# Kernel optimization log

Hardware: AMD Instinct MI355X
Metric: run time of the kernel (lower is better)

Reference implementation:

```python
import jax, jax.numpy as jnp
import numpy as np

N, F_IN, H, OUT, E = 50000, 128, 128, 40, 800000


def setup_inputs() -> dict:
    key = jax.random.key(0)
    ks = jax.random.split(key, 20)
    s = 0.05
    return {
        "x": jax.random.normal(ks[0], (N, F_IN), jnp.float32),
        "edge_index": jax.random.randint(ks[1], (2, E), 0, N, jnp.int64),
        # GATConv (heads=1)
        "W_gat": jax.random.normal(ks[2], (F_IN, H), jnp.float32) * s,
        "att_src": jax.random.normal(ks[3], (H,), jnp.float32) * s,
        "att_dst": jax.random.normal(ks[4], (H,), jnp.float32) * s,
        "b_gat": jnp.zeros((H,), jnp.float32),
        # GCNConv
        "W_gcn": jax.random.normal(ks[5], (F_IN, H), jnp.float32) * s,
        "b_gcn": jnp.zeros((H,), jnp.float32),
        # SAGEConv (mean aggr): lin_l on neighbors (with bias), lin_r on root (no bias)
        "W_sage_l": jax.random.normal(ks[6], (F_IN, H), jnp.float32) * s,
        "b_sage_l": jnp.zeros((H,), jnp.float32),
        "W_sage_r": jax.random.normal(ks[7], (F_IN, H), jnp.float32) * s,
        # MLP head
        "W1": jax.random.normal(ks[8], (3 * H, 2 * H), jnp.float32) * s,
        "b1": jnp.zeros((2 * H,), jnp.float32),
        "W2": jax.random.normal(ks[9], (2 * H, H), jnp.float32) * s,
        "b2": jnp.zeros((H,), jnp.float32),
        "W3": jax.random.normal(ks[10], (H, OUT), jnp.float32) * s,
        "b3": jnp.zeros((OUT,), jnp.float32),
        # BatchNorm1d(3H)
        "gamma": jnp.ones((3 * H,), jnp.float32),
        "beta": jnp.zeros((3 * H,), jnp.float32),
    }


def _add_self_loops(edge_index, n):
    loop = jnp.arange(n, dtype=edge_index.dtype)
    src = jnp.concatenate([edge_index[0], loop])
    dst = jnp.concatenate([edge_index[1], loop])
    return src, dst


def _gat(x, src, dst, n, W, att_src, att_dst, bias):
    h = x @ W                                   # [N, H]
    a_s = h @ att_src                           # [N]
    a_d = h @ att_dst                           # [N]
    e = jax.nn.leaky_relu(a_s[src] + a_d[dst], 0.2)  # [E']
    m = jax.ops.segment_max(e, dst, num_segments=n)
    ex = jnp.exp(e - m[dst])
    denom = jax.ops.segment_sum(ex, dst, num_segments=n)
    alpha = ex / denom[dst]
    out = jax.ops.segment_sum(alpha[:, None] * h[src], dst, num_segments=n)
    return out + bias


def _gcn(x, src, dst, n, W, bias):
    h = x @ W
    deg = jax.ops.segment_sum(jnp.ones_like(dst, dtype=h.dtype), dst, num_segments=n)
    dinv = jnp.where(deg > 0, jax.lax.rsqrt(deg), 0.0)
    norm = dinv[src] * dinv[dst]                # [E']
    out = jax.ops.segment_sum(norm[:, None] * h[src], dst, num_segments=n)
    return out + bias


def _sage(x, src, dst, n, W_l, b_l, W_r):
    agg = jax.ops.segment_sum(x[src], dst, num_segments=n)
    cnt = jax.ops.segment_sum(jnp.ones_like(dst, dtype=x.dtype), dst, num_segments=n)
    mean = agg / jnp.maximum(cnt, 1.0)[:, None]
    return mean @ W_l + b_l + x @ W_r


def reference(x, edge_index, W_gat, att_src, att_dst, b_gat, W_gcn, b_gcn,
              W_sage_l, b_sage_l, W_sage_r, W1, b1, W2, b2, W3, b3, gamma, beta):
    n = x.shape[0]
    src, dst = edge_index[0], edge_index[1]          # SAGE: no self-loops
    src_sl, dst_sl = _add_self_loops(edge_index, n)  # GAT/GCN add self-loops

    x_gat = _gat(x, src_sl, dst_sl, n, W_gat, att_src, att_dst, b_gat)
    x_gcn = _gcn(x, src_sl, dst_sl, n, W_gcn, b_gcn)
    x_sage = _sage(x, src, dst, n, W_sage_l, b_sage_l, W_sage_r)

    h = jnp.concatenate([x_gat, x_gcn, x_sage], axis=1)  # [N, 3H]
    # BatchNorm1d (training-mode batch statistics; biased variance, eps=1e-5)
    mu = h.mean(axis=0)
    var = h.var(axis=0)
    h = (h - mu) * jax.lax.rsqrt(var + 1e-5) * gamma + beta
    # dropout is identity at inference
    h = jax.nn.relu(h) @ W1 + b1
    h = jax.nn.relu(h) @ W2 + b2
    h = jax.nn.relu(h) @ W3 + b3
    return h
```

## Files before the change

kernel.cpp:

```cpp
#include <hip/hip_runtime.h>
#include <cstdint>
#include <cstddef>

#define NN   50000
#define FIN  128
#define HD   128
#define EE   800000
#define C3   384
#define NOUT 40

#define SC_ELEMS 512
#define SC_BLKS  ((NN + SC_ELEMS - 1) / SC_ELEMS)
#define NBLK ((NN + 127) / 128)

#define SPLIT_BLKS ((NN + 4) / 4)

#define NBUCK ((NN + 511) / 512)
#define BCAP  16384
#define BK_BLKS ((EE + 8191) / 8192)
#define SCAP  12288

#define REC_CAP 252
#define ZROW NN

#define LDSW 132

typedef __attribute__((ext_vector_type(8))) short s8v;
typedef __attribute__((ext_vector_type(4))) float f4v;
typedef __attribute__((ext_vector_type(4))) ushort u4v;

typedef const __attribute__((address_space(1))) unsigned int* guintp;
typedef __attribute__((address_space(3))) unsigned int* luintp;

static __device__ __forceinline__ void async_copy16(const void* g, void* l) {
    __builtin_amdgcn_global_load_lds((guintp)g, (luintp)l, 16, 0, 0);
}

static __device__ __forceinline__ float b2f(ushort u) {
    return __uint_as_float((unsigned)u << 16);
}
static __device__ __forceinline__ ushort f2b(float v) {
    unsigned u = __float_as_uint(v);
    unsigned r = u + 0x7fffu + ((u >> 16) & 1u);
    return (ushort)(r >> 16);
}

__global__ __launch_bounds__(256) void k_split_x_att(
    const float* __restrict__ x,
    const float* __restrict__ w_as, const float* __restrict__ w_ad,
    ushort* __restrict__ xb,
    float* __restrict__ a_s, float* __restrict__ a_d)
{
    int node = blockIdx.x * 4 + (threadIdx.x >> 6);
    if (node > NN) return;
    int lane = threadIdx.x & 63;
    size_t o = (size_t)node * 128 + lane * 2;
    if (node == NN) {
        ushort2 z; z.x = 0; z.y = 0;
        *(ushort2*)(xb + o) = z;
        return;
    }
    float2 v  = *(const float2*)(x + o);
    { ushort2 u; u.x = f2b(v.x); u.y = f2b(v.y); *(ushort2*)(xb + o) = u; }
    float2 w1 = *(const float2*)(w_as + lane * 2);
    float2 w2 = *(const float2*)(w_ad + lane * 2);
    float s1 = v.x * w1.x + v.y * w1.y;
    float s2 = v.x * w2.x + v.y * w2.y;
    #pragma unroll
    for (int off = 32; off; off >>= 1) {
        s1 += __shfl_down(s1, off);
        s2 += __shfl_down(s2, off);
    }
    if (lane == 0) { a_s[node] = s1; a_d[node] = s2; }
}

__global__ void k_splitw_all(
    const float* __restrict__ Wg, const float* __restrict__ Wc,
    const float* __restrict__ Wl, const float* __restrict__ Wr,
    const float* __restrict__ W1, const float* __restrict__ W2,
    const float* __restrict__ W3,
    const float* __restrict__ asv, const float* __restrict__ adv,
    float* __restrict__ w_as, float* __restrict__ w_ad,
    ushort* __restrict__ btg, ushort* __restrict__ btc,
    ushort* __restrict__ btsg,
    ushort* __restrict__ bt1, ushort* __restrict__ bt2,
    ushort* __restrict__ bt3)
{
    int ry = blockIdx.x;
    int t = threadIdx.x;
    if (ry == 816) {
        if (t < 128) {
            float s1 = 0.f, s2 = 0.f;
            for (int j = 0; j < 128; ++j) {
                float w = Wg[t * 128 + j];
                s1 += w * asv[j];
                s2 += w * adv[j];
            }
            w_as[t] = s1; w_ad[t] = s2;
        }
        return;
    }
    const float* W = nullptr; ushort* dh; int K, Nw, n;
    bool sage = false;
    if (ry < 128)      { n = ry;       K = 128; Nw = 128; W = Wg; dh = btg; }
    else if (ry < 256) { n = ry - 128; K = 128; Nw = 128; W = Wc; dh = btc; }
    else if (ry < 384) { n = ry - 256; K = 256; Nw = 128; sage = true; dh = btsg; }
    else if (ry < 640) { n = ry - 384; K = 384; Nw = 256; W = W1; dh = bt1; }
    else if (ry < 768) { n = ry - 640; K = 256; Nw = 128; W = W2; dh = bt2; }
    else               { n = ry - 768; K = 128; Nw = 40;  W = W3; dh = bt3; }
    for (int k = t; k < K; k += 256) {
        float v;
        if (sage) v = (k < 128) ? Wl[(size_t)k * 128 + n] : Wr[(size_t)(k - 128) * 128 + n];
        else      v = (n < Nw) ? W[(size_t)k * Nw + n] : 0.f;
        dh[(size_t)n * K + k] = f2b(v);
    }
}

template<int NT, int NCH, int AX>
__global__ __launch_bounds__(256, 5) void k_gemm2(
    const ushort* __restrict__ A, int K,
    const ushort* __restrict__ Bt,
    int M, int mode,
    const float* __restrict__ bias,
    float* __restrict__ Cf, int ldc,
    ushort* __restrict__ Ch, int ldch,
    int colmax)
{
    constexpr int COLS = NT * 16;
    constexpr int HOPU = 8 * COLS;
    constexpr int KTOT = NCH * 128;

    __shared__ __align__(16) ushort S[16384];
    ushort* Bs = S;
    ushort* As = S + 8192;

    const int lane = threadIdx.x & 63;
    const int wave = threadIdx.x >> 6;
    const int quad = lane >> 4;
    const int ln15 = lane & 15;
    const int brow = AX ? blockIdx.y : blockIdx.x;
    const int bcol = AX ? blockIdx.x : blockIdx.y;
    const int row0 = brow * 128 + wave * 32;
    const int col0 = bcol * COLS;
    const int Rbase = brow * 128;

    auto stageB = [&](int c, int h) {
        for (int u0 = wave * 64; u0 < HOPU; u0 += 256) {
            int u  = u0 + lane;
            int kq  = u / COLS;
            int col = u - kq * COLS;
            int kk  = c * 128 + h * 64 + kq * 8;
            const ushort* gp = Bt + (size_t)(col0 + col) * KTOT + kk;
            async_copy16(gp, (char*)Bs + (size_t)u0 * 16);
        }
    };
    auto stageA = [&](int c, int h) {
        #pragma unroll
        for (int i = 0; i < 4; ++i) {
            int u0 = (wave * 4 + i) * 64;
            int u  = u0 + lane;
            int row = u >> 3;
            int s   = u & 7;
            int sg  = s ^ (row & 7);
            int rr = Rbase + row; if (rr > M - 1) rr = M - 1;
            int kk = c * 128 + h * 64 + sg * 8;
            const ushort* gp = A + (size_t)rr * K + kk;
            async_copy16(gp, (char*)As + (size_t)u0 * 16);
        }
    };
    auto afrag = [&](int jj, int mt) -> s8v {
        int r = wave * 32 + mt * 16 + ln15;
        int sg = jj * 4 + quad;
        int unit = r * 8 + (sg ^ (r & 7));
        return *(const s8v*)(As + (size_t)unit * 8);
    };

    f4v acc[2][NT] = {};

    auto compute = [&](int jj) {
        s8v a0 = afrag(jj, 0);
        s8v a1 = afrag(jj, 1);
        #pragma unroll
        for (int t = 0; t < NT; ++t) {
            int ub = (jj * 4 + quad) * COLS + t * 16 + ln15;
            s8v b = *(const s8v*)(Bs + (size_t)ub * 8);
            acc[0][t] = __builtin_amdgcn_mfma_f32_16x16x32_bf16(a0, b, acc[0][t], 0, 0, 0);
            acc[1][t] = __builtin_amdgcn_mfma_f32_16x16x32_bf16(a1, b, acc[1][t], 0, 0, 0);
        }
    };

    stageB(0, 0); stageA(0, 0);
    __syncthreads();

    #pragma unroll
    for (int ph = 0; ph < NCH; ++ph) {
        #pragma unroll
        for (int h = 0; h < 2; ++h) {
            compute(0); compute(1);
            if (!(ph == NCH - 1 && h == 1)) {
                __syncthreads();
                int nc = ph, nh = h + 1;
                if (nh == 2) { nh = 0; ++nc; }
                stageB(nc, nh); stageA(nc, nh);
                __syncthreads();
            }
        }
    }

    if (NT == 8 && mode == 0) {
        __syncthreads();
        ushort* Lp = S + wave * 2176;
        #pragma unroll
        for (int mt = 0; mt < 2; ++mt) {
            #pragma unroll
            for (int t = 0; t < NT; ++t) {
                int cc = col0 + t * 16 + ln15;
                #pragma unroll
                for (int r = 0; r < 4; ++r) {
                    float v = acc[mt][t][r] + bias[cc];
                    v = v > 0.f ? v : 0.f;
                    Lp[(quad * 4 + r) * LDSW + t * 16 + ln15] = f2b(v);
                }
            }
            int cb = (lane & 31) * 4;
            #pragma unroll
            for (int it = 0; it < 8; ++it) {
                int row2 = it * 2 + (lane >> 5);
                int rr = row0 + mt * 16 + row2;
                uint2 v = *(uint2*)(Lp + row2 * LDSW + cb);
                if (rr < M)
                    *(uint2*)(Ch + (size_t)rr * ldch + col0 + cb) = v;
            }
        }
    } else {
        #pragma unroll
        for (int t = 0; t < NT; ++t) {
            int cc = col0 + t * 16 + ln15;
            #pragma unroll
            for (int mt = 0; mt < 2; ++mt) {
                #pragma unroll
                for (int r = 0; r < 4; ++r) {
                    int rr = row0 + mt * 16 + quad * 4 + r;
                    if (rr < M && cc < colmax)
                        Cf[(size_t)rr * ldc + cc] = acc[mt][t][r] + bias[cc];
                }
            }
        }
    }
}

__global__ __launch_bounds__(256, 3) void k_gemm_prod(
    const ushort* __restrict__ tgb, const ushort* __restrict__ tcb,
    const ushort* __restrict__ tsb, const ushort* __restrict__ xb,
    const ushort* __restrict__ btg, const ushort* __restrict__ btc,
    const ushort* __restrict__ btsg,
    const float* __restrict__ bg, const float* __restrict__ bc,
    const float* __restrict__ bsl,
    float* __restrict__ pS, float* __restrict__ pQ,
    ushort* __restrict__ hch)
{
    constexpr int COLS = 128;
    constexpr int HOPU = 8 * COLS;
    __shared__ __align__(16) ushort S[16384];
    ushort* Bs = S;
    ushort* As = S + 8192;
    float* red = (float*)(S + 14336);

    const int z = blockIdx.z;
    const ushort* A1 = (z == 0) ? tgb : (z == 1) ? tcb : tsb;
    const ushort* Bt = (z == 0) ? btg : (z == 1) ? btc : btsg;
    const float*  bias = (z == 0) ? bg : (z == 1) ? bc : bsl;
    const int nch = (z == 2) ? 2 : 1;
    const int ktot = nch * 128;

    const int lane = threadIdx.x & 63;
    const int wave = threadIdx.x >> 6;
    const int quad = lane >> 4;
    const int ln15 = lane & 15;
    const int row0 = blockIdx.x * 128 + wave * 32;
    const int Rbase = blockIdx.x * 128;

    auto stageB = [&](int c, int h) {
        for (int u0 = wave * 64; u0 < HOPU; u0 += 256) {
            int u  = u0 + lane;
            int kq  = u / COLS;
            int col = u - kq * COLS;
            int kk  = c * 128 + h * 64 + kq * 8;
            const ushort* gp = Bt + (size_t)col * ktot + kk;
            async_copy16(gp, (char*)Bs + (size_t)u0 * 16);
        }
    };
    auto stageA = [&](int c, int h) {
        #pragma unroll
        for (int i = 0; i < 4; ++i) {
            int u0 = (wave * 4 + i) * 64;
            int u  = u0 + lane;
            int row = u >> 3;
            int s   = u & 7;
            int sg  = s ^ (row & 7);
            int rr = Rbase + row; if (rr > NN - 1) rr = NN - 1;
            int kk = c * 128 + h * 64 + sg * 8;
            const ushort* gp = (kk < 128) ? (A1 + (size_t)rr * 128 + kk)
                                          : (xb + (size_t)rr * 128 + (kk - 128));
            async_copy16(gp, (char*)As + (size_t)u0 * 16);
        }
    };
    auto afrag = [&](int jj, int mt) -> s8v {
        int r = wave * 32 + mt * 16 + ln15;
        int sg = jj * 4 + quad;
        int unit = r * 8 + (sg ^ (r & 7));
        return *(const s8v*)(As + (size_t)unit * 8);
    };

    f4v acc[2][8] = {};

    auto compute = [&](int jj) {
        s8v a0 = afrag(jj, 0);
        s8v a1 = afrag(jj, 1);
        #pragma unroll
        for (int t = 0; t < 8; ++t) {
            int ub = (jj * 4 + quad) * COLS + t * 16 + ln15;
            s8v b = *(const s8v*)(Bs + (size_t)ub * 8);
            acc[0][t] = __builtin_amdgcn_mfma_f32_16x16x32_bf16(a0, b, acc[0][t], 0, 0, 0);
            acc[1][t] = __builtin_amdgcn_mfma_f32_16x16x32_bf16(a1, b, acc[1][t], 0, 0, 0);
        }
    };

    stageB(0, 0); stageA(0, 0);
    __syncthreads();

    for (int ph = 0; ph < nch; ++ph) {
        for (int h = 0; h < 2; ++h) {
            compute(0); compute(1);
            if (!(ph == nch - 1 && h == 1)) {
                __syncthreads();
                int nc = ph, nh = h + 1;
                if (nh == 2) { nh = 0; ++nc; }
                stageB(nc, nh); stageA(nc, nh);
                __syncthreads();
            }
        }
    }

    __syncthreads();
    if (threadIdx.x < 256) red[threadIdx.x] = 0.f;
    ushort* Lp = S + wave * 2176;
    float sp[8] = {}, qp[8] = {};
    #pragma unroll
    for (int mt = 0; mt < 2; ++mt) {
        #pragma unroll
        for (int t = 0; t < 8; ++t) {
            #pragma unroll
            for (int r = 0; r < 4; ++r) {
                int rr = row0 + mt * 16 + quad * 4 + r;
                float v = acc[mt][t][r] + bias[t * 16 + ln15];
                Lp[(quad * 4 + r) * LDSW + t * 16 + ln15] = f2b(v);
                if (rr < NN) { sp[t] += v; qp[t] += v * v; }
            }
        }
        int cb = (lane & 31) * 4;
        #pragma unroll
        for (int it = 0; it < 8; ++it) {
            int row2 = it * 2 + (lane >> 5);
            int rr = row0 + mt * 16 + row2;
            uint2 v = *(uint2*)(Lp + row2 * LDSW + cb);
            if (rr < NN)
                *(uint2*)(hch + (size_t)rr * C3 + z * 128 + cb) = v;
        }
    }
    __syncthreads();
    #pragma unroll
    for (int t = 0; t < 8; ++t) {
        float s = sp[t], q = qp[t];
        s += __shfl_xor(s, 16); s += __shfl_xor(s, 32);
        q += __shfl_xor(q, 16); q += __shfl_xor(q, 32);
        if (quad == 0) {
            atomicAdd(&red[t * 16 + ln15], s);
            atomicAdd(&red[128 + t * 16 + ln15], q);
        }
    }
    __syncthreads();
    if (threadIdx.x < 128) {
        size_t o = (size_t)blockIdx.x * C3 + z * 128 + threadIdx.x;
        pS[o] = red[threadIdx.x];
        pQ[o] = red[128 + threadIdx.x];
    }
}

__global__ __launch_bounds__(256) void k_scan_part(
    const int* __restrict__ degA, int* __restrict__ bsum)
{
    int t = threadIdx.x;
    int b0 = blockIdx.x * SC_ELEMS;
    int i0 = b0 + t * 2;
    int v0 = (i0 < NN)     ? degA[i0] + 1     : 0;
    int v1 = (i0 + 1 < NN) ? degA[i0 + 1] + 1 : 0;
    int s = v0 + v1;
    #pragma unroll
    for (int off = 32; off; off >>= 1) s += __shfl_down(s, off);
    __shared__ int ws[4];
    if ((t & 63) == 0) ws[t >> 6] = s;
    __syncthreads();
    if (t == 0) bsum[blockIdx.x] = ws[0] + ws[1] + ws[2] + ws[3];
}

__global__ __launch_bounds__(128) void k_scan_tops(
    const int* __restrict__ bsum, int* __restrict__ boffs)
{
    __shared__ int sh[128];
    int t = threadIdx.x;
    int v = (t < SC_BLKS) ? bsum[t] : 0;
    sh[t] = v;
    __syncthreads();
    for (int off = 1; off < 128; off <<= 1) {
        int u = (t >= off) ? sh[t - off] : 0;
        __syncthreads();
        sh[t] += u;
        __syncthreads();
    }
    if (t < SC_BLKS) boffs[t] = sh[t] - v;
    if (t == SC_BLKS - 1) boffs[SC_BLKS] = sh[t];
}

__global__ __launch_bounds__(256) void k_scan_apply(
    const int* __restrict__ degA, const int* __restrict__ boffs,
    int* __restrict__ offs, float* __restrict__ dinv)
{
    __shared__ int sh[256];
    int t = threadIdx.x;
    int b0 = blockIdx.x * SC_ELEMS;
    int i0 = b0 + t * 2;
    int v0 = (i0 < NN)     ? degA[i0] + 1     : 0;
    int v1 = (i0 + 1 < NN) ? degA[i0 + 1] + 1 : 0;
    int pair = v0 + v1;
    sh[t] = pair;
    __syncthreads();
    for (int off = 1; off < 256; off <<= 1) {
        int u = (t >= off) ? sh[t - off] : 0;
        __syncthreads();
        sh[t] += u;
        __syncthreads();
    }
    int excl = sh[t] - pair + boffs[blockIdx.x];
    if (i0 < NN) {
        offs[i0] = excl;
        dinv[i0] = rsqrtf((float)v0);
    }
    if (i0 + 1 < NN) {
        offs[i0 + 1] = excl + v0;
        dinv[i0 + 1] = rsqrtf((float)v1);
    }
    if (blockIdx.x == SC_BLKS - 1 && t == 255) offs[NN] = excl + pair;
}

__global__ __launch_bounds__(1024) void k_bucket(
    const int* __restrict__ e_src, const int* __restrict__ e_dst,
    int* __restrict__ bcnt, uint* __restrict__ ebuf)
{
    __shared__ uint sval[8192];
    __shared__ int scnt[NBUCK], sbase[NBUCK];
    int t = threadIdx.x;
    if (t < NBUCK) scnt[t] = 0;
    __syncthreads();
    int e0 = blockIdx.x * 8192;
    #pragma unroll
    for (int i = 0; i < 8; ++i) {
        int g = e0 + i * 1024 + t;
        uint val = 0xffffffffu;
        if (g < EE) {
            int d = e_dst[g];
            int s = e_src[g];
            int b = d >> 9;
            val = ((uint)b << 25) | ((uint)(d & 511) << 16) | (uint)s;
            atomicAdd(&scnt[b], 1);
        }
        sval[i * 1024 + t] = val;
    }
    __syncthreads();
    if (t < NBUCK) {
        sbase[t] = atomicAdd(&bcnt[t], scnt[t]);
        scnt[t] = 0;
    }
    __syncthreads();
    #pragma unroll
    for (int i = 0; i < 8; ++i) {
        uint val = sval[i * 1024 + t];
        if (val != 0xffffffffu) {
            int b = val >> 25;
            int lo = atomicAdd(&scnt[b], 1);
            ebuf[(size_t)b * BCAP + sbase[b] + lo] = val;
        }
    }
}

__global__ __launch_bounds__(1024) void k_deg(
    const int* __restrict__ bcnt, const uint* __restrict__ ebuf,
    int* __restrict__ degA)
{
    __shared__ int hist[512];
    int b = blockIdx.x, t = threadIdx.x;
    int d0 = b * 512;
    int ndst = NN - d0; if (ndst > 512) ndst = 512;
    if (t < 512) hist[t] = 0;
    __syncthreads();
    int nb = bcnt[b];
    const uint* eb = ebuf + (size_t)b * BCAP;
    for (int i = t; i < nb; i += 1024)
        atomicAdd(&hist[(eb[i] >> 16) & 511], 1);
    __syncthreads();
    if (t < ndst) degA[d0 + t] = hist[t];
}

__global__ __launch_bounds__(1024) void k_csr_build(
    const int* __restrict__ bcnt, const uint* __restrict__ ebuf,
    const int* __restrict__ offs, ushort* __restrict__ esrc)
{
    __shared__ ushort sout[SCAP];
    __shared__ int cur[512];
    int b = blockIdx.x, t = threadIdx.x;
    int d0 = b * 512;
    int ndst = NN - d0; if (ndst > 512) ndst = 512;
    int obase = offs[d0];
    if (t < ndst) cur[t] = offs[d0 + t] - obase;
    __syncthreads();
    int nb = bcnt[b];
    const uint* eb = ebuf + (size_t)b * BCAP;
    for (int i = t; i < nb; i += 1024) {
        uint val = eb[i];
        int slot = atomicAdd(&cur[(val >> 16) & 511], 1);
        sout[slot] = (ushort)(val & 0xffffu);
    }
    if (t < ndst) {
        int slot = atomicAdd(&cur[t], 1);
        sout[slot] = (ushort)(d0 + t);
    }
    __syncthreads();
    int total = offs[d0 + ndst] - obase;
    for (int i = t; i < total; i += 1024)
        esrc[obase + i] = sout[i];
}

__global__ __launch_bounds__(256) void k_gather(
    const ushort* __restrict__ esrc, const int* __restrict__ offs,
    const float* __restrict__ a_s, const float* __restrict__ a_d,
    const float* __restrict__ dinv,
    const ushort* __restrict__ xb,
    ushort* __restrict__ tgb, ushort* __restrict__ tcb,
    ushort* __restrict__ tsb)
{
    __shared__ uint2 recs[4][256];
    int wv = threadIdx.x >> 6;
    int d = blockIdx.x * 4 + wv;
    if (d >= NN) return;
    int lane = threadIdx.x & 63;
    int sub = lane & 31;
    int grp = lane >> 5;
    uint2* rec = recs[wv];
    int beg = offs[d], end = offs[d + 1];
    int cnt = end - beg;
    float ad = a_d[d], dd = dinv[d];
    int stored = cnt < REC_CAP ? cnt : REC_CAP;

    float mloc = -3.0e38f;
    for (int b = 0; b < cnt; b += 64) {
        int j = b + lane;
        int idx = beg + j;
        if (idx < end) {
            int s = esrc[idx];
            float e = a_s[s] + ad;
            e = (e > 0.f) ? e : 0.2f * e;
            mloc = fmaxf(mloc, e);
            if (j < REC_CAP) {
                uint2 r;
                r.x = __float_as_uint(e);
                r.y = (uint)s | ((uint)f2b(dinv[s] * dd) << 16);
                rec[j] = r;
            }
        }
    }
    float m = mloc;
    #pragma unroll
    for (int off = 1; off < 64; off <<= 1) m = fmaxf(m, __shfl_xor(m, off));

    float denl = 0.f;
    for (int j = lane; j < stored; j += 64) {
        float ex = expf(__uint_as_float(rec[j].x) - m);
        denl += ex;
        rec[j].x = __float_as_uint(ex);
    }
    for (int idx = beg + REC_CAP + lane; idx < end; idx += 64) {
        int s = esrc[idx];
        float e = a_s[s] + ad;
        e = (e > 0.f) ? e : 0.2f * e;
        denl += expf(e - m);
    }
    float den = denl;
    #pragma unroll
    for (int off = 1; off < 64; off <<= 1) den += __shfl_xor(den, off);
    float rden = 1.f / den;

    for (int j = lane; j < stored; j += 64) {
        uint2 r = rec[j];
        float wg = __uint_as_float(r.x) * rden;
        uint2 q;
        q.x = (uint)f2b(wg) | (r.y & 0xffff0000u);
        q.y = r.y & 0xffffu;
        rec[j] = q;
    }
    int Pcnt = (stored + 3) & ~3;
    if (lane < Pcnt + 4 - stored) {
        uint2 q; q.x = 0u; q.y = (uint)ZROW;
        rec[stored + lane] = q;
    }

    float tg[4] = {}, tc[4] = {}, ts[4] = {};
    const ushort* xbs = xb + sub * 4;
    auto ldx = [&](uint srow) -> u4v {
        return *(const u4v*)(xbs + (size_t)srow * 128);
    };
    auto fmacc = [&](u4v x4, uint pw) {
        float wg = __uint_as_float(pw << 16);
        float wc = __uint_as_float(pw & 0xffff0000u);
        #pragma unroll
        for (int k = 0; k < 4; ++k) {
            float xv = b2f(x4[k]);
            tg[k] += wg * xv;
            tc[k] += wc * xv;
            ts[k] += xv;
        }
    };

    int mB = Pcnt >> 2;
    uint2 rA0 = rec[grp],     rA1 = rec[2 + grp];
    u4v   xA0 = ldx(rA0.y),   xA1 = ldx(rA1.y);
    uint2 rB0, rB1; u4v xB0, xB1;
    int i = 0;
    for (;;) {
        rB0 = rec[4 * i + 4 + grp]; xB0 = ldx(rB0.y);
        rB1 = rec[4 * i + 6 + grp]; xB1 = ldx(rB1.y);
        fmacc(xA0, rA0.x); fmacc(xA1, rA1.x);
        if (++i >= mB) break;
        rA0 = rec[4 * i + 4 + grp]; xA0 = ldx(rA0.y);
        rA1 = rec[4 * i + 6 + grp]; xA1 = ldx(rA1.y);
        fmacc(xB0, rB0.x); fmacc(xB1, rB1.x);
        if (++i >= mB) break;
    }

    for (int base = beg + REC_CAP; base < end; base += 64) {
        int idx = base + lane;
        int s = ZROW; uint pw = 0;
        if (idx < end) {
            int ss = esrc[idx];
            float e = a_s[ss] + ad;
            e = (e > 0.f) ? e : 0.2f * e;
            pw = (uint)f2b(expf(e - m) * rden) | ((uint)f2b(dinv[ss] * dd) << 16);
            s = ss;
        }
        int cb = end - base; if (cb > 64) cb = 64;
        for (int j = 0; j < cb; j += 2) {
            int jj = j + grp;
            int sa = __shfl(s, jj);
            uint pa = (uint)__shfl((int)pw, jj);
            bool vv = jj < cb;
            sa = vv ? sa : ZROW;
            pa = vv ? pa : 0u;
            fmacc(ldx((uint)sa), pa);
        }
    }

    #pragma unroll
    for (int k = 0; k < 4; ++k) {
        tg[k] += __shfl_xor(tg[k], 32);
        tc[k] += __shfl_xor(tc[k], 32);
        ts[k] += __shfl_xor(ts[k], 32);
    }
    if (lane < 32) {
        u4v xd = *(const u4v*)(xb + (size_t)d * 128 + lane * 4);
        int cs = cnt - 1;
        float rc = 1.f / (float)(cs > 1 ? cs : 1);
        u4v og, oc, os;
        #pragma unroll
        for (int k = 0; k < 4; ++k) {
            og[k] = f2b(tg[k]);
            oc[k] = f2b(tc[k]);
            os[k] = f2b((ts[k] - b2f(xd[k])) * rc);
        }
        size_t row = (size_t)d * 128 + lane * 4;
        *(u4v*)(tgb + row) = og;
        *(u4v*)(tcb + row) = oc;
        *(u4v*)(tsb + row) = os;
    }
}

__global__ void k_bn_final(const float* __restrict__ pS, const float* __restrict__ pQ,
                           const float* __restrict__ gamma, const float* __restrict__ beta,
                           float* __restrict__ scale, float* __restrict__ shift)
{
    int j = blockIdx.x * 64 + threadIdx.x;
    if (j >= C3) return;
    float s = 0.f, q = 0.f;
    for (int r = 0; r < NBLK; ++r) {
        s += pS[(size_t)r * C3 + j];
        q += pQ[(size_t)r * C3 + j];
    }
    const float rn = 1.f / (float)NN;
    float mu  = s * rn;
    float var = q * rn - mu * mu;
    float sc  = gamma[j] * rsqrtf(var + 1e-5f);
    scale[j] = sc;
    shift[j] = beta[j] - mu * sc;
}

__global__ __launch_bounds__(256) void k_bnrelu(
    ushort* __restrict__ hch,
    const float* __restrict__ scale, const float* __restrict__ shift)
{
    int p = blockIdx.x * blockDim.x + threadIdx.x;
    if (p >= NN * 48) return;
    int cidx = (p % 48) * 8;
    size_t o = (size_t)p * 8;
    uint4 w = *(uint4*)(hch + o);
    uint wr[4] = {w.x, w.y, w.z, w.w};
    uint out[4];
    #pragma unroll
    for (int i = 0; i < 4; ++i) {
        ushort u0 = (ushort)(wr[i] & 0xffffu), u1 = (ushort)(wr[i] >> 16);
        int cc = cidx + i * 2;
        float v0 = b2f(u0) * scale[cc]     + shift[cc];
        float v1 = b2f(u1) * scale[cc + 1] + shift[cc + 1];
        v0 = v0 > 0.f ? v0 : 0.f;
        v1 = v1 > 0.f ? v1 : 0.f;
        out[i] = (uint)f2b(v0) | ((uint)f2b(v1) << 16);
    }
    uint4 r; r.x = out[0]; r.y = out[1]; r.z = out[2]; r.w = out[3];
    *(uint4*)(hch + o) = r;
}

extern "C" void kernel_launch(void* const* d_in, const int* in_sizes, int n_in,
                              void* d_out, int out_size, void* d_ws, size_t ws_size,
                              hipStream_t stream) {
    const float* x        = (const float*)d_in[0];
    const int*   ei       = (const int*)d_in[1];
    const float* W_gat    = (const float*)d_in[2];
    const float* att_src  = (const float*)d_in[3];
    const float* att_dst  = (const float*)d_in[4];
    const float* b_gat    = (const float*)d_in[5];
    const float* W_gcn    = (const float*)d_in[6];
    const float* b_gcn    = (const float*)d_in[7];
    const float* W_sage_l = (const float*)d_in[8];
    const float* b_sage_l = (const float*)d_in[9];
    const float* W_sage_r = (const float*)d_in[10];
    const float* W1       = (const float*)d_in[11];
    const float* b1       = (const float*)d_in[12];
    const float* W2       = (const float*)d_in[13];
    const float* b2       = (const float*)d_in[14];
    const float* W3       = (const float*)d_in[15];
    const float* b3       = (const float*)d_in[16];
    const float* gamma    = (const float*)d_in[17];
    const float* beta     = (const float*)d_in[18];

    const int* e_src = ei;
    const int* e_dst = ei + EE;

    char* base = (char*)d_ws;
    size_t o = 0;
    ushort* hch  = (ushort*)(base + o); o += (size_t)NN * C3 * 2;
    ushort* tgb  = (ushort*)(base + o); o += (size_t)NN * 128 * 2;
    ushort* tcb  = (ushort*)(base + o); o += (size_t)NN * 128 * 2;
    ushort* tsb  = (ushort*)(base + o); o += (size_t)NN * 128 * 2;
    ushort* xb   = (ushort*)(base + o); o += (size_t)(NN + 1) * 128 * 2;
    ushort* esrc = (ushort*)(base + o); o += ((size_t)(EE + NN) * 2 + 15) & ~15ull;
    int*    offs = (int*)(base + o);    o += (size_t)(NN + 16) * 4;
    float*  as_  = (float*)(base + o);  o += (size_t)NN * 4;
    float*  ad_  = (float*)(base + o);  o += (size_t)NN * 4;
    float*  dinv = (float*)(base + o);  o += (size_t)NN * 4;
    int*    bsum = (int*)(base + o);    o += 256 * 4;
    int*    boffs= (int*)(base + o);    o += 256 * 4;
    int*    degA = (int*)(base + o);    o += (size_t)NN * 4;
    int*    bcnt = (int*)(base + o);    o += 128 * 4;
    float*  pS   = (float*)(base + o);  o += (size_t)NBLK * C3 * 4;
    float*  pQ   = (float*)(base + o);  o += (size_t)NBLK * C3 * 4;
    float*  scale= (float*)(base + o);  o += C3 * 4;
    float*  shift= (float*)(base + o);  o += C3 * 4;
    float*  w_as = (float*)(base + o);  o += 128 * 4;
    float*  w_ad = (float*)(base + o);  o += 128 * 4;
    ushort* btg  = (ushort*)(base + o); o += 128 * 128 * 2;
    ushort* btc  = (ushort*)(base + o); o += 128 * 128 * 2;
    ushort* btsg = (ushort*)(base + o); o += 128 * 256 * 2;
    ushort* bt1  = (ushort*)(base + o); o += 256 * 384 * 2;
    ushort* bt2  = (ushort*)(base + o); o += 128 * 256 * 2;
    ushort* bt3  = (ushort*)(base + o); o += 48 * 128 * 2;
    ushort* a1 = tgb;
    ushort* a2 = tsb;
    uint*   ebuf = (uint*)hch;

    hipMemsetAsync(bcnt, 0, 128 * 4, stream);

    k_splitw_all<<<817, 256, 0, stream>>>(W_gat, W_gcn, W_sage_l, W_sage_r, W1, W2, W3,
        att_src, att_dst, w_as, w_ad, btg, btc, btsg, bt1, bt2, bt3);
    k_split_x_att<<<SPLIT_BLKS, 256, 0, stream>>>(x, w_as, w_ad, xb, as_, ad_);

    k_bucket<<<BK_BLKS, 1024, 0, stream>>>(e_src, e_dst, bcnt, ebuf);
    k_deg<<<NBUCK, 1024, 0, stream>>>(bcnt, ebuf, degA);
    k_scan_part<<<SC_BLKS, 256, 0, stream>>>(degA, bsum);
    k_scan_tops<<<1, 128, 0, stream>>>(bsum, boffs);
    k_scan_apply<<<SC_BLKS, 256, 0, stream>>>(degA, boffs, offs, dinv);
    k_csr_build<<<NBUCK, 1024, 0, stream>>>(bcnt, ebuf, offs, esrc);

    k_gather<<<(NN + 3) / 4, 256, 0, stream>>>(
        esrc, offs, as_, ad_, dinv, xb, tgb, tcb, tsb);

    k_gemm_prod<<<dim3(NBLK, 1, 3), 256, 0, stream>>>(
        tgb, tcb, tsb, xb, btg, btc, btsg,
        b_gat, b_gcn, b_sage_l, pS, pQ, hch);

    k_bn_final<<<6, 64, 0, stream>>>(pS, pQ, gamma, beta, scale, shift);
    k_bnrelu<<<(NN * 48 + 255) / 256, 256, 0, stream>>>(hch, scale, shift);

    k_gemm2<8, 3, 1><<<dim3(2, NBLK), 256, 0, stream>>>(
        hch, 384, bt1, NN, 0, b1, nullptr, 0, a1, 256, 256);
    k_gemm2<8, 2, 0><<<dim3(NBLK, 1), 256, 0, stream>>>(
        a1, 256, bt2, NN, 0, b2, nullptr, 0, a2, 128, 128);
    k_gemm2<3, 1, 0><<<dim3(NBLK, 1), 256, 0, stream>>>(
        a2, 128, bt3, NN, 2, b3, (float*)d_out, NOUT, nullptr, 0, NOUT);
}
```

Baseline: 335.9 us.

## Fuse degree count with prefix scan and gather with 16 lanes per node

Merges the degree histogram and the three-kernel prefix scan into one kernel. Each bucket block derives its global offset from the bucket edge counts plus node counts, which removes three launches and the degA round trip. The neighbor gather now gives each destination node a 16-lane group instead of a 64-lane wavefront, with 8 bf16 features per lane loaded as 16-byte vectors. This cuts idle lanes for the typical degree of about 17, but nodes above 128 neighbors fall back to a slower serial shuffle path.

Result: faster. 326.5 us (-2.8%).

```diff
diff --git a/kernel.cpp b/kernel.cpp
--- a/kernel.cpp
+++ b/kernel.cpp
@@ -9,8 +9,6 @@
 #define C3   384
 #define NOUT 40
 
-#define SC_ELEMS 512
-#define SC_BLKS  ((NN + SC_ELEMS - 1) / SC_ELEMS)
 #define NBLK ((NN + 127) / 128)
 
 #define SPLIT_BLKS ((NN + 4) / 4)
@@ -20,14 +18,15 @@
 #define BK_BLKS ((EE + 8191) / 8192)
 #define SCAP  12288
 
-#define REC_CAP 252
+#define RCAP      132
+#define STORE_CAP 128
 #define ZROW NN
 
 #define LDSW 132
 
 typedef __attribute__((ext_vector_type(8))) short s8v;
 typedef __attribute__((ext_vector_type(4))) float f4v;
-typedef __attribute__((ext_vector_type(4))) ushort u4v;
+typedef __attribute__((ext_vector_type(8))) ushort u8v;
 
 typedef const __attribute__((address_space(1))) unsigned int* guintp;
 typedef __attribute__((address_space(3))) unsigned int* luintp;
@@ -387,72 +386,6 @@
     }
 }
 
-__global__ __launch_bounds__(256) void k_scan_part(
-    const int* __restrict__ degA, int* __restrict__ bsum)
-{
-    int t = threadIdx.x;
-    int b0 = blockIdx.x * SC_ELEMS;
-    int i0 = b0 + t * 2;
-    int v0 = (i0 < NN)     ? degA[i0] + 1     : 0;
-    int v1 = (i0 + 1 < NN) ? degA[i0 + 1] + 1 : 0;
-    int s = v0 + v1;
-    #pragma unroll
-    for (int off = 32; off; off >>= 1) s += __shfl_down(s, off);
-    __shared__ int ws[4];
-    if ((t & 63) == 0) ws[t >> 6] = s;
-    __syncthreads();
-    if (t == 0) bsum[blockIdx.x] = ws[0] + ws[1] + ws[2] + ws[3];
-}
-
-__global__ __launch_bounds__(128) void k_scan_tops(
-    const int* __restrict__ bsum, int* __restrict__ boffs)
-{
-    __shared__ int sh[128];
-    int t = threadIdx.x;
-    int v = (t < SC_BLKS) ? bsum[t] : 0;
-    sh[t] = v;
-    __syncthreads();
-    for (int off = 1; off < 128; off <<= 1) {
-        int u = (t >= off) ? sh[t - off] : 0;
-        __syncthreads();
-        sh[t] += u;
-        __syncthreads();
-    }
-    if (t < SC_BLKS) boffs[t] = sh[t] - v;
-    if (t == SC_BLKS - 1) boffs[SC_BLKS] = sh[t];
-}
-
-__global__ __launch_bounds__(256) void k_scan_apply(
-    const int* __restrict__ degA, const int* __restrict__ boffs,
-    int* __restrict__ offs, float* __restrict__ dinv)
-{
-    __shared__ int sh[256];
-    int t = threadIdx.x;
-    int b0 = blockIdx.x * SC_ELEMS;
-    int i0 = b0 + t * 2;
-    int v0 = (i0 < NN)     ? degA[i0] + 1     : 0;
-    int v1 = (i0 + 1 < NN) ? degA[i0 + 1] + 1 : 0;
-    int pair = v0 + v1;
-    sh[t] = pair;
-    __syncthreads();
-    for (int off = 1; off < 256; off <<= 1) {
-        int u = (t >= off) ? sh[t - off] : 0;
-        __syncthreads();
-        sh[t] += u;
-        __syncthreads();
-    }
-    int excl = sh[t] - pair + boffs[blockIdx.x];
-    if (i0 < NN) {
-        offs[i0] = excl;
-        dinv[i0] = rsqrtf((float)v0);
-    }
-    if (i0 + 1 < NN) {
-        offs[i0 + 1] = excl + v0;
-        dinv[i0 + 1] = rsqrtf((float)v1);
-    }
-    if (blockIdx.x == SC_BLKS - 1 && t == 255) offs[NN] = excl + pair;
-}
-
 __global__ __launch_bounds__(1024) void k_bucket(
     const int* __restrict__ e_src, const int* __restrict__ e_dst,
     int* __restrict__ bcnt, uint* __restrict__ ebuf)
@@ -493,14 +426,15 @@
     }
 }
 
-__global__ __launch_bounds__(1024) void k_deg(
+__global__ __launch_bounds__(1024) void k_degscan(
     const int* __restrict__ bcnt, const uint* __restrict__ ebuf,
-    int* __restrict__ degA)
+    int* __restrict__ offs, float* __restrict__ dinv)
 {
     __shared__ int hist[512];
+    __shared__ int sh[256];
+    __shared__ int btop;
     int b = blockIdx.x, t = threadIdx.x;
     int d0 = b * 512;
-    int ndst = NN - d0; if (ndst > 512) ndst = 512;
     if (t < 512) hist[t] = 0;
     __syncthreads();
     int nb = bcnt[b];
@@ -508,7 +442,39 @@
     for (int i = t; i < nb; i += 1024)
         atomicAdd(&hist[(eb[i] >> 16) & 511], 1);
     __syncthreads();
-    if (t < ndst) degA[d0 + t] = hist[t];
+    if (t < 64) {
+        int acc = 0;
+        for (int i = t; i < b; i += 64) {
+            int nd = NN - i * 512; if (nd > 512) nd = 512;
+            acc += bcnt[i] + nd;
+        }
+        #pragma unroll
+        for (int off = 32; off; off >>= 1) acc += __shfl_down(acc, off);
+        if (t == 0) btop = acc;
+    }
+    int v0 = 0, v1 = 0;
+    if (t < 256) {
+        int i0g = d0 + t * 2;
+        v0 = (i0g < NN) ? hist[t * 2] + 1 : 0;
+        v1 = (i0g + 1 < NN) ? hist[t * 2 + 1] + 1 : 0;
+        sh[t] = v0 + v1;
+    }
+    __syncthreads();
+    for (int off = 1; off < 256; off <<= 1) {
+        int u = 0;
+        if (t < 256 && t >= off) u = sh[t - off];
+        __syncthreads();
+        if (t < 256) sh[t] += u;
+        __syncthreads();
+    }
+    if (t < 256) {
+        int pair = v0 + v1;
+        int excl = sh[t] - pair + btop;
+        int i0g = d0 + t * 2;
+        if (i0g < NN)     { offs[i0g] = excl;          dinv[i0g] = rsqrtf((float)v0); }
+        if (i0g + 1 < NN) { offs[i0g + 1] = excl + v0; dinv[i0g + 1] = rsqrtf((float)v1); }
+        if (b == NBUCK - 1 && t == 255) offs[NN] = excl + pair;
+    }
 }
 
 __global__ __launch_bounds__(1024) void k_csr_build(
@@ -548,29 +514,27 @@
     ushort* __restrict__ tgb, ushort* __restrict__ tcb,
     ushort* __restrict__ tsb)
 {
-    __shared__ uint2 recs[4][256];
-    int wv = threadIdx.x >> 6;
-    int d = blockIdx.x * 4 + wv;
+    __shared__ uint2 recs[16][RCAP];
+    int t = threadIdx.x;
+    int qid = t >> 4;
+    int ln = t & 15;
+    int d = blockIdx.x * 16 + qid;
     if (d >= NN) return;
-    int lane = threadIdx.x & 63;
-    int sub = lane & 31;
-    int grp = lane >> 5;
-    uint2* rec = recs[wv];
+    uint2* rec = recs[qid];
     int beg = offs[d], end = offs[d + 1];
     int cnt = end - beg;
     float ad = a_d[d], dd = dinv[d];
-    int stored = cnt < REC_CAP ? cnt : REC_CAP;
+    int stored = cnt < STORE_CAP ? cnt : STORE_CAP;
 
     float mloc = -3.0e38f;
-    for (int b = 0; b < cnt; b += 64) {
-        int j = b + lane;
-        int idx = beg + j;
-        if (idx < end) {
-            int s = esrc[idx];
+    for (int b = 0; b < cnt; b += 16) {
+        int j = b + ln;
+        if (j < cnt) {
+            int s = esrc[beg + j];
             float e = a_s[s] + ad;
             e = (e > 0.f) ? e : 0.2f * e;
             mloc = fmaxf(mloc, e);
-            if (j < REC_CAP) {
+            if (j < STORE_CAP) {
                 uint2 r;
                 r.x = __float_as_uint(e);
                 r.y = (uint)s | ((uint)f2b(dinv[s] * dd) << 16);
@@ -580,15 +544,15 @@
     }
     float m = mloc;
     #pragma unroll
-    for (int off = 1; off < 64; off <<= 1) m = fmaxf(m, __shfl_xor(m, off));
+    for (int off = 1; off < 16; off <<= 1) m = fmaxf(m, __shfl_xor(m, off, 16));
 
     float denl = 0.f;
-    for (int j = lane; j < stored; j += 64) {
+    for (int j = ln; j < stored; j += 16) {
         float ex = expf(__uint_as_float(rec[j].x) - m);
         denl += ex;
         rec[j].x = __float_as_uint(ex);
     }
-    for (int idx = beg + REC_CAP + lane; idx < end; idx += 64) {
+    for (int idx = beg + STORE_CAP + ln; idx < end; idx += 16) {
         int s = esrc[idx];
         float e = a_s[s] + ad;
         e = (e > 0.f) ? e : 0.2f * e;
@@ -596,58 +560,50 @@
     }
     float den = denl;
     #pragma unroll
-    for (int off = 1; off < 64; off <<= 1) den += __shfl_xor(den, off);
+    for (int off = 1; off < 16; off <<= 1) den += __shfl_xor(den, off, 16);
     float rden = 1.f / den;
 
-    for (int j = lane; j < stored; j += 64) {
+    for (int j = ln; j < stored; j += 16) {
         uint2 r = rec[j];
-        float wg = __uint_as_float(r.x) * rden;
         uint2 q;
-        q.x = (uint)f2b(wg) | (r.y & 0xffff0000u);
+        q.x = (uint)f2b(__uint_as_float(r.x) * rden) | (r.y & 0xffff0000u);
         q.y = r.y & 0xffffu;
         rec[j] = q;
     }
-    int Pcnt = (stored + 3) & ~3;
-    if (lane < Pcnt + 4 - stored) {
-        uint2 q; q.x = 0u; q.y = (uint)ZROW;
-        rec[stored + lane] = q;
-    }
-
-    float tg[4] = {}, tc[4] = {}, ts[4] = {};
-    const ushort* xbs = xb + sub * 4;
-    auto ldx = [&](uint srow) -> u4v {
-        return *(const u4v*)(xbs + (size_t)srow * 128);
-    };
-    auto fmacc = [&](u4v x4, uint pw) {
+    if (ln < 2) { uint2 q; q.x = 0u; q.y = (uint)ZROW; rec[stored + ln] = q; }
+
+    float tg[8] = {}, tc[8] = {}, ts[8] = {};
+    const ushort* xbs = xb + ln * 8;
+    auto ldx = [&](uint srow) -> u8v {
+        return *(const u8v*)(xbs + (size_t)srow * 128);
+    };
+    auto fmacc = [&](u8v x8, uint pw) {
         float wg = __uint_as_float(pw << 16);
         float wc = __uint_as_float(pw & 0xffff0000u);
         #pragma unroll
-        for (int k = 0; k < 4; ++k) {
-            float xv = b2f(x4[k]);
+        for (int k = 0; k < 8; ++k) {
+            float xv = b2f(x8[k]);
             tg[k] += wg * xv;
             tc[k] += wc * xv;
             ts[k] += xv;
         }
     };
 
-    int mB = Pcnt >> 2;
-    uint2 rA0 = rec[grp],     rA1 = rec[2 + grp];
-    u4v   xA0 = ldx(rA0.y),   xA1 = ldx(rA1.y);
-    uint2 rB0, rB1; u4v xB0, xB1;
-    int i = 0;
+    int Pcnt = (stored + 1) & ~1;
+    uint2 rA = rec[0]; u8v xA = ldx(rA.y);
+    uint2 rB; u8v xB;
+    int j = 0;
     for (;;) {
-        rB0 = rec[4 * i + 4 + grp]; xB0 = ldx(rB0.y);
-        rB1 = rec[4 * i + 6 + grp]; xB1 = ldx(rB1.y);
-        fmacc(xA0, rA0.x); fmacc(xA1, rA1.x);
-        if (++i >= mB) break;
-        rA0 = rec[4 * i + 4 + grp]; xA0 = ldx(rA0.y);
-        rA1 = rec[4 * i + 6 + grp]; xA1 = ldx(rA1.y);
-        fmacc(xB0, rB0.x); fmacc(xB1, rB1.x);
-        if (++i >= mB) break;
-    }
-
-    for (int base = beg + REC_CAP; base < end; base += 64) {
-        int idx = base + lane;
+        rB = rec[j + 1]; xB = ldx(rB.y);
+        fmacc(xA, rA.x);
+        if (++j >= Pcnt) break;
+        rA = rec[j + 1]; xA = ldx(rA.y);
+        fmacc(xB, rB.x);
+        if (++j >= Pcnt) break;
+    }
+
+    for (int base = beg + STORE_CAP; base < end; base += 16) {
+        int idx = base + ln;
         int s = ZROW; uint pw = 0;
         if (idx < end) {
             int ss = esrc[idx];
@@ -656,40 +612,28 @@
             pw = (uint)f2b(expf(e - m) * rden) | ((uint)f2b(dinv[ss] * dd) << 16);
             s = ss;
         }
-        int cb = end - base; if (cb > 64) cb = 64;
-        for (int j = 0; j < cb; j += 2) {
-            int jj = j + grp;
-            int sa = __shfl(s, jj);
-            uint pa = (uint)__shfl((int)pw, jj);
-            bool vv = jj < cb;
-            sa = vv ? sa : ZROW;
-            pa = vv ? pa : 0u;
+        int cb = end - base; if (cb > 16) cb = 16;
+        for (int jj = 0; jj < cb; ++jj) {
+            int sa = __shfl(s, jj, 16);
+            uint pa = (uint)__shfl((int)pw, jj, 16);
             fmacc(ldx((uint)sa), pa);
         }
     }
 
-    #pragma unroll
-    for (int k = 0; k < 4; ++k) {
-        tg[k] += __shfl_xor(tg[k], 32);
-        tc[k] += __shfl_xor(tc[k], 32);
-        ts[k] += __shfl_xor(ts[k], 32);
-    }
-    if (lane < 32) {
-        u4v xd = *(const u4v*)(xb + (size_t)d * 128 + lane * 4);
-        int cs = cnt - 1;
-        float rc = 1.f / (float)(cs > 1 ? cs : 1);
-        u4v og, oc, os;
-        #pragma unroll
-        for (int k = 0; k < 4; ++k) {
-            og[k] = f2b(tg[k]);
-            oc[k] = f2b(tc[k]);
-            os[k] = f2b((ts[k] - b2f(xd[k])) * rc);
-        }
-        size_t row = (size_t)d * 128 + lane * 4;
-        *(u4v*)(tgb + row) = og;
-        *(u4v*)(tcb + row) = oc;
-        *(u4v*)(tsb + row) = os;
-    }
+    u8v xd = *(const u8v*)(xb + (size_t)d * 128 + ln * 8);
+    int cs = cnt - 1;
+    float rc = 1.f / (float)(cs > 1 ? cs : 1);
+    u8v og, oc, os;
+    #pragma unroll
+    for (int k = 0; k < 8; ++k) {
+        og[k] = f2b(tg[k]);
+        oc[k] = f2b(tc[k]);
+        os[k] = f2b((ts[k] - b2f(xd[k])) * rc);
+    }
+    size_t row = (size_t)d * 128 + ln * 8;
+    *(u8v*)(tgb + row) = og;
+    *(u8v*)(tcb + row) = oc;
+    *(u8v*)(tsb + row) = os;
 }
 
 __global__ void k_bn_final(const float* __restrict__ pS, const float* __restrict__ pQ,
@@ -774,9 +718,6 @@
     float*  as_  = (float*)(base + o);  o += (size_t)NN * 4;
     float*  ad_  = (float*)(base + o);  o += (size_t)NN * 4;
     float*  dinv = (float*)(base + o);  o += (size_t)NN * 4;
-    int*    bsum = (int*)(base + o);    o += 256 * 4;
-    int*    boffs= (int*)(base + o);    o += 256 * 4;
-    int*    degA = (int*)(base + o);    o += (size_t)NN * 4;
     int*    bcnt = (int*)(base + o);    o += 128 * 4;
     float*  pS   = (float*)(base + o);  o += (size_t)NBLK * C3 * 4;
     float*  pQ   = (float*)(base + o);  o += (size_t)NBLK * C3 * 4;
@@ -801,13 +742,10 @@
     k_split_x_att<<<SPLIT_BLKS, 256, 0, stream>>>(x, w_as, w_ad, xb, as_, ad_);
 
     k_bucket<<<BK_BLKS, 1024, 0, stream>>>(e_src, e_dst, bcnt, ebuf);
-    k_deg<<<NBUCK, 1024, 0, stream>>>(bcnt, ebuf, degA);
-    k_scan_part<<<SC_BLKS, 256, 0, stream>>>(degA, bsum);
-    k_scan_tops<<<1, 128, 0, stream>>>(bsum, boffs);
-    k_scan_apply<<<SC_BLKS, 256, 0, stream>>>(degA, boffs, offs, dinv);
+    k_degscan<<<NBUCK, 1024, 0, stream>>>(bcnt, ebuf, offs, dinv);
     k_csr_build<<<NBUCK, 1024, 0, stream>>>(bcnt, ebuf, offs, esrc);
 
-    k_gather<<<(NN + 3) / 4, 256, 0, stream>>>(
+    k_gather<<<(NN + 15) / 16, 256, 0, stream>>>(
         esrc, offs, as_, ad_, dinv, xb, tgb, tcb, tsb);
 
     k_gemm_prod<<<dim3(NBLK, 1, 3), 256, 0, stream>>>(
```
